# Kernel tuning notes

Hardware: AMD Instinct MI355X
Metric: run time of the kernel (lower is better)

Reference implementation:

```python
import jax, jax.numpy as jnp
import numpy as np

GROUPS = 32
EPS = 1e-5


def setup_inputs() -> dict:
    key = jax.random.key(0)
    ks = jax.random.split(key, 4)
    B, C, H, W = 4, 256, 64, 64
    x = jax.random.normal(ks[0], (B, C, H, W), dtype=jnp.float32)
    gn_w = jnp.ones((C,), jnp.float32)
    gn_b = jnp.zeros((C,), jnp.float32)
    qkv_w = jax.random.normal(ks[1], (3 * C, C), dtype=jnp.float32) * (C ** -0.5)
    qkv_b = jnp.zeros((3 * C,), jnp.float32)
    proj_w = jax.random.normal(ks[2], (C, C), dtype=jnp.float32) * (C ** -0.5)
    proj_b = jnp.zeros((C,), jnp.float32)
    return {"x": x, "gn_w": gn_w, "gn_b": gn_b, "qkv_w": qkv_w,
            "qkv_b": qkv_b, "proj_w": proj_w, "proj_b": proj_b}


def _group_norm(x, w, b):
    B, C, H, W = x.shape
    xr = x.reshape(B, GROUPS, -1)                      # [B, G, (C/G)*H*W]
    mean = xr.mean(axis=-1, keepdims=True)
    var = xr.var(axis=-1, keepdims=True)               # biased, like torch
    h = ((xr - mean) * jax.lax.rsqrt(var + EPS)).reshape(B, C, H, W)
    return h * w[None, :, None, None] + b[None, :, None, None]


def reference(x, gn_w, gn_b, qkv_w, qkv_b, proj_w, proj_b):
    B, C, H, W = x.shape
    h = _group_norm(x, gn_w, gn_b)
    # 1x1 conv == channel GEMM
    qkv = jnp.einsum('oc,bchw->bohw', qkv_w, h) + qkv_b[None, :, None, None]
    qkv = qkv.reshape(B, 3, C, H * W)
    q, k, v = qkv[:, 0], qkv[:, 1], qkv[:, 2]          # [B, C, N]
    scale = C ** (-0.5)
    attn = jax.nn.softmax(jnp.einsum('bci,bcj->bij', q, k) * scale, axis=-1)
    out = jnp.einsum('bij,bcj->bci', attn, v).reshape(B, C, H, W)
    out = jnp.einsum('oc,bchw->bohw', proj_w, out) + proj_b[None, :, None, None]
    return x + out
```

## Files before the change

### kernel.cpp

```cpp
#include <hip/hip_runtime.h>
#include <hip/hip_bf16.h>
#include <math.h>

typedef __bf16 bf16;
typedef __bf16 bf16x8 __attribute__((ext_vector_type(8)));
typedef __bf16 bf16x4 __attribute__((ext_vector_type(4)));
typedef float f32x4 __attribute__((ext_vector_type(4)));
typedef float f32x16 __attribute__((ext_vector_type(16)));

#define MFMA16(a, b, c) __builtin_amdgcn_mfma_f32_16x16x32_bf16(a, b, c, 0, 0, 0)
#define MFMA32(a, b, c) __builtin_amdgcn_mfma_f32_32x32x16_bf16(a, b, c, 0, 0, 0)

#define SCALEK 0.09016844005555896f

typedef const __attribute__((address_space(1))) void* gas_t;
typedef __attribute__((address_space(3))) void* las_t;

__global__ __launch_bounds__(256) void gn_kernel(
    const float* __restrict__ x, const float* __restrict__ gw,
    const float* __restrict__ gb, bf16* __restrict__ h) {
  const int bg = blockIdx.x;
  const int b = bg >> 5, g = bg & 31;
  const size_t base = (size_t)(b * 256 + g * 8) * 4096;
  const float* xp = x + base;
  bf16* hp = h + base;
  const int tid = threadIdx.x;

  float s = 0.f, ss = 0.f;
  for (int i = tid * 4; i < 32768; i += 1024) {
    float4 v = *(const float4*)(xp + i);
    s += v.x + v.y + v.z + v.w;
    ss += v.x * v.x + v.y * v.y + v.z * v.z + v.w * v.w;
  }
#pragma unroll
  for (int off = 32; off; off >>= 1) {
    s += __shfl_down(s, off);
    ss += __shfl_down(ss, off);
  }
  __shared__ float red[8];
  if ((tid & 63) == 0) {
    red[(tid >> 6) * 2] = s;
    red[(tid >> 6) * 2 + 1] = ss;
  }
  __syncthreads();
  s = red[0] + red[2] + red[4] + red[6];
  ss = red[1] + red[3] + red[5] + red[7];
  const float mean = s * (1.f / 32768.f);
  const float var = ss * (1.f / 32768.f) - mean * mean;
  const float rstd = rsqrtf(var + 1e-5f);

  for (int i = tid * 4; i < 32768; i += 1024) {
    float4 v = *(const float4*)(xp + i);
    int c = g * 8 + (i >> 12);
    float a = gw[c] * rstd;
    float b2 = gb[c] - mean * a;
    bf16x4 o;
    o[0] = (bf16)(v.x * a + b2);
    o[1] = (bf16)(v.y * a + b2);
    o[2] = (bf16)(v.z * a + b2);
    o[3] = (bf16)(v.w * a + b2);
    *(bf16x4*)(hp + i) = o;
  }
}

__global__ __launch_bounds__(256) void qkv_gemm(
    const bf16* __restrict__ h, const float* __restrict__ w,
    const float* __restrict__ bias, bf16* __restrict__ qt,
    bf16* __restrict__ kt, bf16* __restrict__ vcm) {
  const int b = blockIdx.z;
  const int o0 = blockIdx.y * 64;
  const int p0 = blockIdx.x * 64;
  __shared__ bf16 Alds[64][56];
  __shared__ bf16 Blds[64][56];
  const int tid = threadIdx.x;
  const int lane = tid & 63, wid = tid >> 6;
  const int lr = lane & 15, lg = lane >> 4;
  const int wm = wid >> 1, wn = wid & 1;
  const bf16* hb = h + (size_t)b * 256 * 4096;

  f32x4 acc[2][2] = {};

  for (int k0 = 0; k0 < 256; k0 += 32) {
    {
      int row = tid >> 2, c8 = (tid & 3) * 8;
      const float* src = w + (size_t)(o0 + row) * 256 + k0 + c8;
      float4 v0 = *(const float4*)src;
      float4 v1 = *(const float4*)(src + 4);
      bf16x8 bv;
      bv[0] = (bf16)v0.x; bv[1] = (bf16)v0.y; bv[2] = (bf16)v0.z; bv[3] = (bf16)v0.w;
      bv[4] = (bf16)v1.x; bv[5] = (bf16)v1.y; bv[6] = (bf16)v1.z; bv[7] = (bf16)v1.w;
      *(bf16x8*)&Alds[row][c8] = bv;
    }
    {
      int cc = tid >> 3, p8 = (tid & 7) * 8;
      bf16x8 v = *(const bf16x8*)(hb + (size_t)(k0 + cc) * 4096 + p0 + p8);
#pragma unroll
      for (int e = 0; e < 8; ++e) Blds[p8 + e][cc] = v[e];
    }
    __syncthreads();
    bf16x8 af[2], bfr[2];
#pragma unroll
    for (int mi = 0; mi < 2; ++mi)
      af[mi] = *(const bf16x8*)&Alds[wm * 32 + mi * 16 + lr][lg * 8];
#pragma unroll
    for (int ni = 0; ni < 2; ++ni)
      bfr[ni] = *(const bf16x8*)&Blds[wn * 32 + ni * 16 + lr][lg * 8];
#pragma unroll
    for (int mi = 0; mi < 2; ++mi)
#pragma unroll
      for (int ni = 0; ni < 2; ++ni)
        acc[mi][ni] = MFMA16(af[mi], bfr[ni], acc[mi][ni]);
    __syncthreads();
  }

#pragma unroll
  for (int mi = 0; mi < 2; ++mi) {
#pragma unroll
    for (int ni = 0; ni < 2; ++ni) {
#pragma unroll
      for (int r = 0; r < 4; ++r) {
        int o = o0 + wm * 32 + mi * 16 + lg * 4 + r;
        int p = p0 + wn * 32 + ni * 16 + lr;
        float val = acc[mi][ni][r] + bias[o];
        if (o < 256) {
          qt[((size_t)b * 4096 + p) * 256 + o] = (bf16)val;
        } else if (o < 512) {
          kt[((size_t)b * 4096 + p) * 256 + (o - 256)] = (bf16)(val * SCALEK);
        } else {
          vcm[((size_t)b * 256 + (o - 512)) * 4096 + p] = (bf16)val;
        }
      }
    }
  }
}

template <int S>
__global__ __launch_bounds__(256, 2) void flash_attn(
    const bf16* __restrict__ qt, const bf16* __restrict__ kt,
    const bf16* __restrict__ vcm, bf16* __restrict__ Opart,
    float* __restrict__ l_g) {
  constexpr int NCOMBO = 4 * S;
  constexpr int CSH = (S == 4) ? 4 : (S == 2) ? 3 : 2;
  constexpr int NIT = (4096 / S) / 32;
  const int bid = blockIdx.x;
  const int combo = bid & (NCOMBO - 1);
  const int qtile = bid >> CSH;
  const int b = combo & 3;
  const int split = combo >> 2;
  const int i0 = qtile * 128;
  const int jbase = split * (4096 / S);

  __shared__ bf16 Klds[2][32][256];
  __shared__ bf16 Vlds[2][256][32];
  const int tid = threadIdx.x;
  const int lane = tid & 63, w = tid >> 6;
  const int ln = lane & 31;
  const int hv = lane >> 5;
  const bf16* qb = qt + (size_t)b * 4096 * 256;
  const bf16* kb = kt + (size_t)b * 4096 * 256;
  const bf16* vb = vcm + (size_t)b * 256 * 4096;

  const int qrow = i0 + w * 32 + ln;
  bf16x8 qf[16];
#pragma unroll
  for (int ks = 0; ks < 16; ++ks)
    qf[ks] = *(const bf16x8*)(qb + (size_t)qrow * 256 + ks * 16 + hv * 8);

  int koff[4], voff[4];
#pragma unroll
  for (int it = 0; it < 4; ++it) {
    int chunk = tid + 256 * it;
    int krow = chunk >> 5;
    koff[it] = krow * 256 + ((((chunk & 31) ^ (krow & 7)) * 8));
    int vrow = chunk >> 2;
    voff[it] = vrow * 4096 + (((chunk & 3) ^ (vrow & 3)) * 8);
  }

#define STAGE(JT, BUF)                                                        \
  {                                                                           \
    const int j0s = jbase + (JT) * 32;                                        \
    _Pragma("unroll") for (int it = 0; it < 4; ++it) {                        \
      int chunk = tid + 256 * it;                                             \
      __builtin_amdgcn_global_load_lds(                                       \
          (gas_t)(const void*)(kb + (size_t)j0s * 256 + koff[it]),            \
          (las_t)(void*)(&Klds[BUF][0][0] + chunk * 8), 16, 0, 0);            \
      __builtin_amdgcn_global_load_lds(                                       \
          (gas_t)(const void*)(vb + (size_t)j0s + voff[it]),                  \
          (las_t)(void*)(&Vlds[BUF][0][0] + chunk * 8), 16, 0, 0);            \
    }                                                                         \
  }

  float llane = 0.f;
  f32x16 accO[8] = {};
  const int kswz = ln & 7;
  const int vswz = ln & 3;

  STAGE(0, 0);
  asm volatile("s_waitcnt vmcnt(0)" ::: "memory");
  __builtin_amdgcn_s_barrier();

  for (int jt = 0; jt < NIT; ++jt) {
    const int cur = jt & 1;
    if (jt + 1 < NIT) STAGE(jt + 1, cur ^ 1);

    f32x16 a0 = {}, a1 = {};
    __builtin_amdgcn_s_setprio(1);
#pragma unroll
    for (int ks = 0; ks < 8; ++ks) {
      bf16x8 kf0 =
          *(const bf16x8*)&Klds[cur][ln][((2 * ks + hv) ^ kswz) * 8];
      bf16x8 kf1 =
          *(const bf16x8*)&Klds[cur][ln][((2 * (ks + 8) + hv) ^ kswz) * 8];
      a0 = MFMA32(kf0, qf[ks], a0);
      a1 = MFMA32(kf1, qf[ks + 8], a1);
    }
    __builtin_amdgcn_s_setprio(0);

    float pv[16];
#pragma unroll
    for (int r = 0; r < 16; ++r) pv[r] = exp2f(a0[r] + a1[r]);
    llane += (((pv[0] + pv[1]) + (pv[2] + pv[3])) +
              ((pv[4] + pv[5]) + (pv[6] + pv[7]))) +
             (((pv[8] + pv[9]) + (pv[10] + pv[11])) +
              ((pv[12] + pv[13]) + (pv[14] + pv[15])));

    int pk[8];
#pragma unroll
    for (int q4 = 0; q4 < 8; ++q4)
      asm("v_cvt_pk_bf16_f32 %0, %1, %2"
          : "=v"(pk[q4])
          : "v"(pv[q4 * 2]), "v"(pv[q4 * 2 + 1]));
    bf16x8 pfrag[2];
#pragma unroll
    for (int s = 0; s < 2; ++s) {
      int xa = pk[s * 4 + 0], ya = pk[s * 4 + 2];
      int xb = pk[s * 4 + 1], yb = pk[s * 4 + 3];
      asm("v_permlane32_swap_b32 %0, %1" : "+v"(xa), "+v"(ya));
      asm("v_permlane32_swap_b32 %0, %1" : "+v"(xb), "+v"(yb));
      union { int i[4]; bf16x8 v; } u;
      u.i[0] = xa; u.i[1] = xb; u.i[2] = ya; u.i[3] = yb;
      pfrag[s] = u.v;
    }

    __builtin_amdgcn_s_setprio(1);
#pragma unroll
    for (int s = 0; s < 2; ++s) {
#pragma unroll
      for (int cb = 0; cb < 8; ++cb) {
        bf16x8 vf =
            *(const bf16x8*)&Vlds[cur][cb * 32 + ln][((2 * s + hv) ^ vswz) * 8];
        accO[cb] = MFMA32(vf, pfrag[s], accO[cb]);
      }
    }
    __builtin_amdgcn_s_setprio(0);

    asm volatile("s_waitcnt vmcnt(0)" ::: "memory");
    __builtin_amdgcn_s_barrier();
  }
#undef STAGE

  bf16* ob = Opart + ((size_t)(split * 4 + b) * 4096 + qrow) * 256;
#pragma unroll
  for (int cb = 0; cb < 8; ++cb) {
#pragma unroll
    for (int g = 0; g < 4; ++g) {
      int lo, hi;
      asm("v_cvt_pk_bf16_f32 %0, %1, %2"
          : "=v"(lo)
          : "v"(accO[cb][g * 4 + 0]), "v"(accO[cb][g * 4 + 1]));
      asm("v_cvt_pk_bf16_f32 %0, %1, %2"
          : "=v"(hi)
          : "v"(accO[cb][g * 4 + 2]), "v"(accO[cb][g * 4 + 3]));
      int2 val; val.x = lo; val.y = hi;
      *(int2*)(ob + cb * 32 + g * 8 + hv * 4) = val;
    }
  }
  {
    int xa = __float_as_int(llane);
    int ya = xa;
    asm("v_permlane32_swap_b32 %0, %1" : "+v"(xa), "+v"(ya));
    float ltot = __int_as_float(xa) + __int_as_float(ya);
    if (hv == 0)
      l_g[(size_t)(split * 4 + b) * 4096 + qrow] = ltot;
  }
}

template <int S>
__global__ __launch_bounds__(256) void merge_kernel(
    const bf16* __restrict__ Opart, const float* __restrict__ l_g,
    bf16* __restrict__ att) {
  int idx = blockIdx.x * 256 + threadIdx.x;
  int row = idx >> 5, c8 = (idx & 31) * 8;
  float L = 0.f;
#pragma unroll
  for (int s = 0; s < S; ++s) L += l_g[s * 16384 + row];
  float acc[8] = {};
#pragma unroll
  for (int s = 0; s < S; ++s) {
    bf16x8 o = *(const bf16x8*)(Opart + ((size_t)s * 16384 + row) * 256 + c8);
#pragma unroll
    for (int e = 0; e < 8; ++e) acc[e] += (float)o[e];
  }
  float inv = 1.f / L;
  bf16x8 res;
#pragma unroll
  for (int e = 0; e < 8; ++e) res[e] = (bf16)(acc[e] * inv);
  *(bf16x8*)(att + (size_t)row * 256 + c8) = res;
}

__global__ __launch_bounds__(256) void proj_gemm(
    const bf16* __restrict__ att, const float* __restrict__ w,
    const float* __restrict__ bias, const float* __restrict__ x,
    float* __restrict__ out) {
  const int b = blockIdx.z;
  const int o0 = blockIdx.y * 64;
  const int p0 = blockIdx.x * 64;
  __shared__ bf16 Alds[64][56];
  __shared__ bf16 Blds[64][56];
  const int tid = threadIdx.x;
  const int lane = tid & 63, wid = tid >> 6;
  const int lr = lane & 15, lg = lane >> 4;
  const int wm = wid >> 1, wn = wid & 1;
  const bf16* ab = att + (size_t)b * 4096 * 256;

  f32x4 acc[2][2] = {};

  for (int k0 = 0; k0 < 256; k0 += 32) {
    {
      int row = tid >> 2, c8 = (tid & 3) * 8;
      const float* src = w + (size_t)(o0 + row) * 256 + k0 + c8;
      float4 v0 = *(const float4*)src;
      float4 v1 = *(const float4*)(src + 4);
      bf16x8 bv;
      bv[0] = (bf16)v0.x; bv[1] = (bf16)v0.y; bv[2] = (bf16)v0.z; bv[3] = (bf16)v0.w;
      bv[4] = (bf16)v1.x; bv[5] = (bf16)v1.y; bv[6] = (bf16)v1.z; bv[7] = (bf16)v1.w;
      *(bf16x8*)&Alds[row][c8] = bv;
    }
    {
      int pr = tid >> 2, c8 = (tid & 3) * 8;
      *(bf16x8*)&Blds[pr][c8] =
          *(const bf16x8*)(ab + (size_t)(p0 + pr) * 256 + k0 + c8);
    }
    __syncthreads();
    bf16x8 af[2], bfr[2];
#pragma unroll
    for (int mi = 0; mi < 2; ++mi)
      af[mi] = *(const bf16x8*)&Alds[wm * 32 + mi * 16 + lr][lg * 8];
#pragma unroll
    for (int ni = 0; ni < 2; ++ni)
      bfr[ni] = *(const bf16x8*)&Blds[wn * 32 + ni * 16 + lr][lg * 8];
#pragma unroll
    for (int mi = 0; mi < 2; ++mi)
#pragma unroll
      for (int ni = 0; ni < 2; ++ni)
        acc[mi][ni] = MFMA16(af[mi], bfr[ni], acc[mi][ni]);
    __syncthreads();
  }

#pragma unroll
  for (int mi = 0; mi < 2; ++mi) {
#pragma unroll
    for (int ni = 0; ni < 2; ++ni) {
#pragma unroll
      for (int r = 0; r < 4; ++r) {
        int o = o0 + wm * 32 + mi * 16 + lg * 4 + r;
        int p = p0 + wn * 32 + ni * 16 + lr;
        size_t idx = ((size_t)b * 256 + o) * 4096 + p;
        out[idx] = acc[mi][ni][r] + bias[o] + x[idx];
      }
    }
  }
}

extern "C" void kernel_launch(void* const* d_in, const int* in_sizes, int n_in,
                              void* d_out, int out_size, void* d_ws,
                              size_t ws_size, hipStream_t stream) {
  (void)in_sizes; (void)n_in; (void)out_size;
  const float* x = (const float*)d_in[0];
  const float* gn_w = (const float*)d_in[1];
  const float* gn_b = (const float*)d_in[2];
  const float* qkv_w = (const float*)d_in[3];
  const float* qkv_b = (const float*)d_in[4];
  const float* proj_w = (const float*)d_in[5];
  const float* proj_b = (const float*)d_in[6];
  float* out = (float*)d_out;

  const size_t MB = 1024ull * 1024ull;
  char* ws = (char*)d_ws;
  bf16* h = (bf16*)(ws);
  bf16* qt = (bf16*)(ws + 8 * MB);
  bf16* kt = (bf16*)(ws + 16 * MB);
  bf16* vcm = (bf16*)(ws + 24 * MB);

  int S;
  if (ws_size >= 32 * MB + 4 * 8 * MB + 4ull * 16384 * sizeof(float)) S = 4;
  else if (ws_size >= 32 * MB + 2 * 8 * MB + 2ull * 16384 * sizeof(float)) S = 2;
  else S = 1;

  bf16* Opart;
  float* l_g;
  bf16* att = h;
  if (S >= 2) {
    Opart = (bf16*)(ws + 32 * MB);
    l_g = (float*)(ws + 32 * MB + (size_t)S * 8 * MB);
  } else {
    Opart = h;
    l_g = (float*)(ws + 32 * MB);
  }

  gn_kernel<<<128, 256, 0, stream>>>(x, gn_w, gn_b, h);
  qkv_gemm<<<dim3(64, 12, 4), 256, 0, stream>>>(h, qkv_w, qkv_b, qt, kt, vcm);
  if (S == 4) {
    flash_attn<4><<<32 * 16, 256, 0, stream>>>(qt, kt, vcm, Opart, l_g);
    merge_kernel<4><<<2048, 256, 0, stream>>>(Opart, l_g, att);
  } else if (S == 2) {
    flash_attn<2><<<32 * 8, 256, 0, stream>>>(qt, kt, vcm, Opart, l_g);
    merge_kernel<2><<<2048, 256, 0, stream>>>(Opart, l_g, att);
  } else {
    flash_attn<1><<<32 * 4, 256, 0, stream>>>(qt, kt, vcm, Opart, l_g);
    merge_kernel<1><<<2048, 256, 0, stream>>>(Opart, l_g, att);
  }
  proj_gemm<<<dim3(64, 4, 4), 256, 0, stream>>>(att, proj_w, proj_b, x, out);
}
```

Measured before the change: 188.8 us.

## Split key tiles across warp pairs in flash attention and fuse merge into projection

Flash attention now uses 64-query tiles. Each pair of warps splits a 64-key tile, and the partial outputs are reduced through LDS at the end. Double-buffered K/V staging is replaced by single buffers whose next-tile loads are issued right after each buffer is consumed, with waits placed between the phases. The separate merge kernel is removed: the projection GEMM now sums the split partials and normalizes by the row sums while loading its B operand. This cuts a kernel launch and the round trip of the merged attention output, in exchange for more blocks, extra barriers and the LDS reduction.

```diff
diff --git a/kernel.cpp b/kernel.cpp
--- a/kernel.cpp
+++ b/kernel.cpp
@@ -141,80 +141,94 @@
     float* __restrict__ l_g) {
   constexpr int NCOMBO = 4 * S;
   constexpr int CSH = (S == 4) ? 4 : (S == 2) ? 3 : 2;
-  constexpr int NIT = (4096 / S) / 32;
+  constexpr int NIT = (4096 / S) / 64;
   const int bid = blockIdx.x;
   const int combo = bid & (NCOMBO - 1);
   const int qtile = bid >> CSH;
   const int b = combo & 3;
   const int split = combo >> 2;
-  const int i0 = qtile * 128;
+  const int i0 = qtile * 64;
   const int jbase = split * (4096 / S);
 
-  __shared__ bf16 Klds[2][32][256];
-  __shared__ bf16 Vlds[2][256][32];
+  __shared__ bf16 Klds[64][256];
+  __shared__ bf16 Vlds[256][64];
+  __shared__ float lred[2][2][32];
   const int tid = threadIdx.x;
   const int lane = tid & 63, w = tid >> 6;
+  const int qg = w >> 1, jg = w & 1;
   const int ln = lane & 31;
   const int hv = lane >> 5;
   const bf16* qb = qt + (size_t)b * 4096 * 256;
   const bf16* kb = kt + (size_t)b * 4096 * 256;
   const bf16* vb = vcm + (size_t)b * 256 * 4096;
 
-  const int qrow = i0 + w * 32 + ln;
+  const int qrow = i0 + qg * 32 + ln;
   bf16x8 qf[16];
 #pragma unroll
   for (int ks = 0; ks < 16; ++ks)
     qf[ks] = *(const bf16x8*)(qb + (size_t)qrow * 256 + ks * 16 + hv * 8);
-
-  int koff[4], voff[4];
-#pragma unroll
-  for (int it = 0; it < 4; ++it) {
+  asm volatile("s_waitcnt vmcnt(0)" ::: "memory");
+
+  int koff[8], voff[8];
+#pragma unroll
+  for (int it = 0; it < 8; ++it) {
     int chunk = tid + 256 * it;
     int krow = chunk >> 5;
-    koff[it] = krow * 256 + ((((chunk & 31) ^ (krow & 7)) * 8));
-    int vrow = chunk >> 2;
-    voff[it] = vrow * 4096 + (((chunk & 3) ^ (vrow & 3)) * 8);
-  }
-
-#define STAGE(JT, BUF)                                                        \
+    int kslot = (chunk & 31) ^ (krow & 7);
+    koff[it] = krow * 256 + kslot * 8;
+    int vrow = chunk >> 3;
+    int vslot = (chunk & 7) ^ (vrow & 7);
+    voff[it] = vrow * 4096 + vslot * 8;
+  }
+
+#define STAGE_K(JT)                                                           \
   {                                                                           \
-    const int j0s = jbase + (JT) * 32;                                        \
-    _Pragma("unroll") for (int it = 0; it < 4; ++it) {                        \
+    const bf16* kbt = kb + (size_t)(jbase + (JT) * 64) * 256;                 \
+    _Pragma("unroll") for (int it = 0; it < 8; ++it) {                        \
       int chunk = tid + 256 * it;                                             \
       __builtin_amdgcn_global_load_lds(                                       \
-          (gas_t)(const void*)(kb + (size_t)j0s * 256 + koff[it]),            \
-          (las_t)(void*)(&Klds[BUF][0][0] + chunk * 8), 16, 0, 0);            \
+          (gas_t)(const void*)(kbt + koff[it]),                               \
+          (las_t)(void*)(&Klds[0][0] + chunk * 8), 16, 0, 0);                 \
+    }                                                                         \
+  }
+#define STAGE_V(JT)                                                           \
+  {                                                                           \
+    const bf16* vbt = vb + (size_t)(jbase + (JT) * 64);                       \
+    _Pragma("unroll") for (int it = 0; it < 8; ++it) {                        \
+      int chunk = tid + 256 * it;                                             \
       __builtin_amdgcn_global_load_lds(                                       \
-          (gas_t)(const void*)(vb + (size_t)j0s + voff[it]),                  \
-          (las_t)(void*)(&Vlds[BUF][0][0] + chunk * 8), 16, 0, 0);            \
+          (gas_t)(const void*)(vbt + voff[it]),                               \
+          (las_t)(void*)(&Vlds[0][0] + chunk * 8), 16, 0, 0);                 \
     }                                                                         \
   }
 
   float llane = 0.f;
   f32x16 accO[8] = {};
-  const int kswz = ln & 7;
-  const int vswz = ln & 3;
-
-  STAGE(0, 0);
-  asm volatile("s_waitcnt vmcnt(0)" ::: "memory");
-  __builtin_amdgcn_s_barrier();
+  const int kk = ln & 7;
+
+  STAGE_K(0);
+  STAGE_V(0);
 
   for (int jt = 0; jt < NIT; ++jt) {
-    const int cur = jt & 1;
-    if (jt + 1 < NIT) STAGE(jt + 1, cur ^ 1);
+    asm volatile("s_waitcnt vmcnt(8)" ::: "memory");
+    __builtin_amdgcn_s_barrier();
+    __builtin_amdgcn_sched_barrier(0);
 
     f32x16 a0 = {}, a1 = {};
     __builtin_amdgcn_s_setprio(1);
 #pragma unroll
     for (int ks = 0; ks < 8; ++ks) {
       bf16x8 kf0 =
-          *(const bf16x8*)&Klds[cur][ln][((2 * ks + hv) ^ kswz) * 8];
+          *(const bf16x8*)&Klds[jg * 32 + ln][((2 * ks + hv) ^ kk) * 8];
       bf16x8 kf1 =
-          *(const bf16x8*)&Klds[cur][ln][((2 * (ks + 8) + hv) ^ kswz) * 8];
+          *(const bf16x8*)&Klds[jg * 32 + ln][((2 * (ks + 8) + hv) ^ kk) * 8];
       a0 = MFMA32(kf0, qf[ks], a0);
       a1 = MFMA32(kf1, qf[ks + 8], a1);
     }
     __builtin_amdgcn_s_setprio(0);
+
+    __builtin_amdgcn_s_barrier();
+    if (jt + 1 < NIT) STAGE_K(jt + 1);
 
     float pv[16];
 #pragma unroll
@@ -223,7 +237,6 @@
               ((pv[4] + pv[5]) + (pv[6] + pv[7]))) +
              (((pv[8] + pv[9]) + (pv[10] + pv[11])) +
               ((pv[12] + pv[13]) + (pv[14] + pv[15])));
-
     int pk[8];
 #pragma unroll
     for (int q4 = 0; q4 < 8; ++q4)
@@ -242,86 +255,122 @@
       pfrag[s] = u.v;
     }
 
+    if (jt + 1 < NIT) {
+      asm volatile("s_waitcnt vmcnt(8)" ::: "memory");
+    } else {
+      asm volatile("s_waitcnt vmcnt(0)" ::: "memory");
+    }
+    __builtin_amdgcn_s_barrier();
+    __builtin_amdgcn_sched_barrier(0);
+
     __builtin_amdgcn_s_setprio(1);
 #pragma unroll
     for (int s = 0; s < 2; ++s) {
 #pragma unroll
       for (int cb = 0; cb < 8; ++cb) {
-        bf16x8 vf =
-            *(const bf16x8*)&Vlds[cur][cb * 32 + ln][((2 * s + hv) ^ vswz) * 8];
+        bf16x8 vf = *(const bf16x8*)&Vlds[cb * 32 + ln]
+                                        [((jg * 4 + s * 2 + hv) ^ kk) * 8];
         accO[cb] = MFMA32(vf, pfrag[s], accO[cb]);
       }
     }
     __builtin_amdgcn_s_setprio(0);
 
-    asm volatile("s_waitcnt vmcnt(0)" ::: "memory");
     __builtin_amdgcn_s_barrier();
-  }
-#undef STAGE
-
-  bf16* ob = Opart + ((size_t)(split * 4 + b) * 4096 + qrow) * 256;
-#pragma unroll
-  for (int cb = 0; cb < 8; ++cb) {
-#pragma unroll
-    for (int g = 0; g < 4; ++g) {
-      int lo, hi;
-      asm("v_cvt_pk_bf16_f32 %0, %1, %2"
-          : "=v"(lo)
-          : "v"(accO[cb][g * 4 + 0]), "v"(accO[cb][g * 4 + 1]));
-      asm("v_cvt_pk_bf16_f32 %0, %1, %2"
-          : "=v"(hi)
-          : "v"(accO[cb][g * 4 + 2]), "v"(accO[cb][g * 4 + 3]));
-      int2 val; val.x = lo; val.y = hi;
-      *(int2*)(ob + cb * 32 + g * 8 + hv * 4) = val;
-    }
-  }
+    if (jt + 1 < NIT) STAGE_V(jt + 1);
+  }
+#undef STAGE_K
+#undef STAGE_V
+
   {
-    int xa = __float_as_int(llane);
-    int ya = xa;
+    int xa = __float_as_int(llane), ya = xa;
     asm("v_permlane32_swap_b32 %0, %1" : "+v"(xa), "+v"(ya));
-    float ltot = __int_as_float(xa) + __int_as_float(ya);
-    if (hv == 0)
-      l_g[(size_t)(split * 4 + b) * 4096 + qrow] = ltot;
+    llane = __int_as_float(xa) + __int_as_float(ya);
+  }
+  if (hv == 0) lred[qg][jg][ln] = llane;
+
+  float* R = (qg == 0) ? (float*)&Klds[0][0] : (float*)&Vlds[0][0];
+#pragma unroll
+  for (int h = 0; h < 2; ++h) {
+    __syncthreads();
+    if (jg == 1) {
+#pragma unroll
+      for (int cb = 0; cb < 4; ++cb) {
+#pragma unroll
+        for (int g = 0; g < 4; ++g) {
+          f32x4 v;
+          v[0] = accO[h * 4 + cb][g * 4 + 0];
+          v[1] = accO[h * 4 + cb][g * 4 + 1];
+          v[2] = accO[h * 4 + cb][g * 4 + 2];
+          v[3] = accO[h * 4 + cb][g * 4 + 3];
+          *(f32x4*)(R + ln * 132 + cb * 32 + g * 8 + hv * 4) = v;
+        }
+      }
+    }
+    __syncthreads();
+    if (jg == 0) {
+#pragma unroll
+      for (int cb = 0; cb < 4; ++cb) {
+#pragma unroll
+        for (int g = 0; g < 4; ++g) {
+          f32x4 v = *(const f32x4*)(R + ln * 132 + cb * 32 + g * 8 + hv * 4);
+          accO[h * 4 + cb][g * 4 + 0] += v[0];
+          accO[h * 4 + cb][g * 4 + 1] += v[1];
+          accO[h * 4 + cb][g * 4 + 2] += v[2];
+          accO[h * 4 + cb][g * 4 + 3] += v[3];
+        }
+      }
+    }
+  }
+  __syncthreads();
+
+  if (jg == 0) {
+    bf16* ob = Opart + ((size_t)(split * 4 + b) * 4096 + qrow) * 256;
+#pragma unroll
+    for (int cb = 0; cb < 8; ++cb) {
+#pragma unroll
+      for (int g = 0; g < 4; ++g) {
+        int lo, hi;
+        asm("v_cvt_pk_bf16_f32 %0, %1, %2"
+            : "=v"(lo)
+            : "v"(accO[cb][g * 4 + 0]), "v"(accO[cb][g * 4 + 1]));
+        asm("v_cvt_pk_bf16_f32 %0, %1, %2"
+            : "=v"(hi)
+            : "v"(accO[cb][g * 4 + 2]), "v"(accO[cb][g * 4 + 3]));
+        int2 val; val.x = lo; val.y = hi;
+        *(int2*)(ob + cb * 32 + g * 8 + hv * 4) = val;
+      }
+    }
+    if (hv == 0) {
+      float lt = lred[qg][0][ln] + lred[qg][1][ln];
+      l_g[(size_t)(split * 4 + b) * 4096 + qrow] = lt;
+    }
   }
 }
 
 template <int S>
-__global__ __launch_bounds__(256) void merge_kernel(
+__global__ __launch_bounds__(256) void proj_fused(
     const bf16* __restrict__ Opart, const float* __restrict__ l_g,
-    bf16* __restrict__ att) {
-  int idx = blockIdx.x * 256 + threadIdx.x;
-  int row = idx >> 5, c8 = (idx & 31) * 8;
-  float L = 0.f;
-#pragma unroll
-  for (int s = 0; s < S; ++s) L += l_g[s * 16384 + row];
-  float acc[8] = {};
-#pragma unroll
-  for (int s = 0; s < S; ++s) {
-    bf16x8 o = *(const bf16x8*)(Opart + ((size_t)s * 16384 + row) * 256 + c8);
-#pragma unroll
-    for (int e = 0; e < 8; ++e) acc[e] += (float)o[e];
-  }
-  float inv = 1.f / L;
-  bf16x8 res;
-#pragma unroll
-  for (int e = 0; e < 8; ++e) res[e] = (bf16)(acc[e] * inv);
-  *(bf16x8*)(att + (size_t)row * 256 + c8) = res;
-}
-
-__global__ __launch_bounds__(256) void proj_gemm(
-    const bf16* __restrict__ att, const float* __restrict__ w,
-    const float* __restrict__ bias, const float* __restrict__ x,
-    float* __restrict__ out) {
+    const float* __restrict__ w, const float* __restrict__ bias,
+    const float* __restrict__ x, float* __restrict__ out) {
   const int b = blockIdx.z;
   const int o0 = blockIdx.y * 64;
   const int p0 = blockIdx.x * 64;
   __shared__ bf16 Alds[64][56];
   __shared__ bf16 Blds[64][56];
+  __shared__ float Linv[64];
   const int tid = threadIdx.x;
   const int lane = tid & 63, wid = tid >> 6;
   const int lr = lane & 15, lg = lane >> 4;
   const int wm = wid >> 1, wn = wid & 1;
-  const bf16* ab = att + (size_t)b * 4096 * 256;
+
+  if (tid < 64) {
+    float L = 0.f;
+#pragma unroll
+    for (int s = 0; s < S; ++s)
+      L += l_g[(size_t)(s * 4 + b) * 4096 + p0 + tid];
+    Linv[tid] = 1.f / L;
+  }
+  __syncthreads();
 
   f32x4 acc[2][2] = {};
 
@@ -338,8 +387,19 @@
     }
     {
       int pr = tid >> 2, c8 = (tid & 3) * 8;
-      *(bf16x8*)&Blds[pr][c8] =
-          *(const bf16x8*)(ab + (size_t)(p0 + pr) * 256 + k0 + c8);
+      float a8[8] = {};
+#pragma unroll
+      for (int s = 0; s < S; ++s) {
+        bf16x8 o = *(const bf16x8*)(
+            Opart + ((size_t)(s * 4 + b) * 4096 + p0 + pr) * 256 + k0 + c8);
+#pragma unroll
+        for (int e = 0; e < 8; ++e) a8[e] += (float)o[e];
+      }
+      float inv = Linv[pr];
+      bf16x8 bv;
+#pragma unroll
+      for (int e = 0; e < 8; ++e) bv[e] = (bf16)(a8[e] * inv);
+      *(bf16x8*)&Blds[pr][c8] = bv;
     }
     __syncthreads();
     bf16x8 af[2], bfr[2];
@@ -397,28 +457,22 @@
   else if (ws_size >= 32 * MB + 2 * 8 * MB + 2ull * 16384 * sizeof(float)) S = 2;
   else S = 1;
 
-  bf16* Opart;
-  float* l_g;
-  bf16* att = h;
-  if (S >= 2) {
-    Opart = (bf16*)(ws + 32 * MB);
-    l_g = (float*)(ws + 32 * MB + (size_t)S * 8 * MB);
-  } else {
-    Opart = h;
-    l_g = (float*)(ws + 32 * MB);
-  }
+  bf16* Opart = (bf16*)(ws + 32 * MB);
+  float* l_g = (float*)(ws + 32 * MB + (size_t)S * 8 * MB);
 
   gn_kernel<<<128, 256, 0, stream>>>(x, gn_w, gn_b, h);
   qkv_gemm<<<dim3(64, 12, 4), 256, 0, stream>>>(h, qkv_w, qkv_b, qt, kt, vcm);
   if (S == 4) {
-    flash_attn<4><<<32 * 16, 256, 0, stream>>>(qt, kt, vcm, Opart, l_g);
-    merge_kernel<4><<<2048, 256, 0, stream>>>(Opart, l_g, att);
+    flash_attn<4><<<64 * 16, 256, 0, stream>>>(qt, kt, vcm, Opart, l_g);
+    proj_fused<4><<<dim3(64, 4, 4), 256, 0, stream>>>(Opart, l_g, proj_w,
+                                                      proj_b, x, out);
   } else if (S == 2) {
-    flash_attn<2><<<32 * 8, 256, 0, stream>>>(qt, kt, vcm, Opart, l_g);
-    merge_kernel<2><<<2048, 256, 0, stream>>>(Opart, l_g, att);
+    flash_attn<2><<<64 * 8, 256, 0, stream>>>(qt, kt, vcm, Opart, l_g);
+    proj_fused<2><<<dim3(64, 4, 4), 256, 0, stream>>>(Opart, l_g, proj_w,
+                                                      proj_b, x, out);
   } else {
-    flash_attn<1><<<32 * 4, 256, 0, stream>>>(qt, kt, vcm, Opart, l_g);
-    merge_kernel<1><<<2048, 256, 0, stream>>>(Opart, l_g, att);
-  }
-  proj_gemm<<<dim3(64, 4, 4), 256, 0, stream>>>(att, proj_w, proj_b, x, out);
+    flash_attn<1><<<64 * 4, 256, 0, stream>>>(qt, kt, vcm, Opart, l_g);
+    proj_fused<1><<<dim3(64, 4, 4), 256, 0, stream>>>(Opart, l_g, proj_w,
+                                                      proj_b, x, out);
+  }
 }
```

Measured after the change: 215.7 us. +14.2%, slower.

## Software-pipeline QK with PV in flash attention and fuse split merge into projection

Applied to the files above, without the earlier changes.

The attention loop is restructured so the QK^T MFMAs for the next key tile interleave with the PV MFMAs of the current tile. K and V staging are split so K runs two tiles ahead and V one tile ahead, with a single wait and barrier at the top of each iteration. The separate merge kernel is removed: the projection GEMM now sums the split partial outputs and divides by the summed row normalisers while loading its B tile. This drops a kernel launch and an intermediate round trip through memory, but the projection repeats the split reduction for each of its four output-channel blocks and holds more registers in the attention loop.

```diff
diff --git a/kernel.cpp b/kernel.cpp
--- a/kernel.cpp
+++ b/kernel.cpp
@@ -176,7 +176,7 @@
     voff[it] = vrow * 4096 + (((chunk & 3) ^ (vrow & 3)) * 8);
   }
 
-#define STAGE(JT, BUF)                                                        \
+#define STAGE_K(JT, BUF)                                                      \
   {                                                                           \
     const int j0s = jbase + (JT) * 32;                                        \
     _Pragma("unroll") for (int it = 0; it < 4; ++it) {                        \
@@ -184,6 +184,13 @@
       __builtin_amdgcn_global_load_lds(                                       \
           (gas_t)(const void*)(kb + (size_t)j0s * 256 + koff[it]),            \
           (las_t)(void*)(&Klds[BUF][0][0] + chunk * 8), 16, 0, 0);            \
+    }                                                                         \
+  }
+#define STAGE_V(JT, BUF)                                                      \
+  {                                                                           \
+    const int j0s = jbase + (JT) * 32;                                        \
+    _Pragma("unroll") for (int it = 0; it < 4; ++it) {                        \
+      int chunk = tid + 256 * it;                                             \
       __builtin_amdgcn_global_load_lds(                                       \
           (gas_t)(const void*)(vb + (size_t)j0s + voff[it]),                  \
           (las_t)(void*)(&Vlds[BUF][0][0] + chunk * 8), 16, 0, 0);            \
@@ -195,26 +202,28 @@
   const int kswz = ln & 7;
   const int vswz = ln & 3;
 
-  STAGE(0, 0);
+  STAGE_K(0, 0);
+  STAGE_V(0, 0);
   asm volatile("s_waitcnt vmcnt(0)" ::: "memory");
   __builtin_amdgcn_s_barrier();
 
-  for (int jt = 0; jt < NIT; ++jt) {
-    const int cur = jt & 1;
-    if (jt + 1 < NIT) STAGE(jt + 1, cur ^ 1);
-
-    f32x16 a0 = {}, a1 = {};
-    __builtin_amdgcn_s_setprio(1);
-#pragma unroll
-    for (int ks = 0; ks < 8; ++ks) {
-      bf16x8 kf0 =
-          *(const bf16x8*)&Klds[cur][ln][((2 * ks + hv) ^ kswz) * 8];
-      bf16x8 kf1 =
-          *(const bf16x8*)&Klds[cur][ln][((2 * (ks + 8) + hv) ^ kswz) * 8];
-      a0 = MFMA32(kf0, qf[ks], a0);
-      a1 = MFMA32(kf1, qf[ks + 8], a1);
-    }
-    __builtin_amdgcn_s_setprio(0);
+  f32x16 a0 = {}, a1 = {};
+#pragma unroll
+  for (int ks = 0; ks < 8; ++ks) {
+    bf16x8 kf0 = *(const bf16x8*)&Klds[0][ln][((2 * ks + hv) ^ kswz) * 8];
+    bf16x8 kf1 =
+        *(const bf16x8*)&Klds[0][ln][((2 * (ks + 8) + hv) ^ kswz) * 8];
+    a0 = MFMA32(kf0, qf[ks], a0);
+    a1 = MFMA32(kf1, qf[ks + 8], a1);
+  }
+  STAGE_K(1, 1);
+
+  for (int t = 0; t < NIT; ++t) {
+    asm volatile("s_waitcnt vmcnt(0)" ::: "memory");
+    __builtin_amdgcn_s_barrier();
+
+    if (t + 1 < NIT) STAGE_V(t + 1, (t + 1) & 1);
+    if (t + 2 < NIT) STAGE_K(t + 2, t & 1);
 
     float pv[16];
 #pragma unroll
@@ -242,22 +251,38 @@
       pfrag[s] = u.v;
     }
 
+    const bf16(*Kc)[256] = Klds[(t + 1) & 1];
+    const bf16(*Vc)[32] = Vlds[t & 1];
     __builtin_amdgcn_s_setprio(1);
-#pragma unroll
-    for (int s = 0; s < 2; ++s) {
-#pragma unroll
-      for (int cb = 0; cb < 8; ++cb) {
-        bf16x8 vf =
-            *(const bf16x8*)&Vlds[cur][cb * 32 + ln][((2 * s + hv) ^ vswz) * 8];
-        accO[cb] = MFMA32(vf, pfrag[s], accO[cb]);
+    if (t + 1 < NIT) {
+      f32x16 n0 = {}, n1 = {};
+#pragma unroll
+      for (int u = 0; u < 8; ++u) {
+        bf16x8 kf0 = *(const bf16x8*)&Kc[ln][((2 * u + hv) ^ kswz) * 8];
+        n0 = MFMA32(kf0, qf[u], n0);
+        bf16x8 kf1 =
+            *(const bf16x8*)&Kc[ln][((2 * (u + 8) + hv) ^ kswz) * 8];
+        n1 = MFMA32(kf1, qf[u + 8], n1);
+        bf16x8 vf0 = *(const bf16x8*)&Vc[u * 32 + ln][((hv) ^ vswz) * 8];
+        accO[u] = MFMA32(vf0, pfrag[0], accO[u]);
+        bf16x8 vf1 = *(const bf16x8*)&Vc[u * 32 + ln][((2 + hv) ^ vswz) * 8];
+        accO[u] = MFMA32(vf1, pfrag[1], accO[u]);
       }
+      a0 = n0;
+      a1 = n1;
+    } else {
+#pragma unroll
+      for (int u = 0; u < 8; ++u) {
+        bf16x8 vf0 = *(const bf16x8*)&Vc[u * 32 + ln][((hv) ^ vswz) * 8];
+        accO[u] = MFMA32(vf0, pfrag[0], accO[u]);
+        bf16x8 vf1 = *(const bf16x8*)&Vc[u * 32 + ln][((2 + hv) ^ vswz) * 8];
+        accO[u] = MFMA32(vf1, pfrag[1], accO[u]);
+      }
     }
     __builtin_amdgcn_s_setprio(0);
-
-    asm volatile("s_waitcnt vmcnt(0)" ::: "memory");
-    __builtin_amdgcn_s_barrier();
-  }
-#undef STAGE
+  }
+#undef STAGE_K
+#undef STAGE_V
 
   bf16* ob = Opart + ((size_t)(split * 4 + b) * 4096 + qrow) * 256;
 #pragma unroll
@@ -286,42 +311,29 @@
 }
 
 template <int S>
-__global__ __launch_bounds__(256) void merge_kernel(
+__global__ __launch_bounds__(256) void proj_fused(
     const bf16* __restrict__ Opart, const float* __restrict__ l_g,
-    bf16* __restrict__ att) {
-  int idx = blockIdx.x * 256 + threadIdx.x;
-  int row = idx >> 5, c8 = (idx & 31) * 8;
-  float L = 0.f;
-#pragma unroll
-  for (int s = 0; s < S; ++s) L += l_g[s * 16384 + row];
-  float acc[8] = {};
-#pragma unroll
-  for (int s = 0; s < S; ++s) {
-    bf16x8 o = *(const bf16x8*)(Opart + ((size_t)s * 16384 + row) * 256 + c8);
-#pragma unroll
-    for (int e = 0; e < 8; ++e) acc[e] += (float)o[e];
-  }
-  float inv = 1.f / L;
-  bf16x8 res;
-#pragma unroll
-  for (int e = 0; e < 8; ++e) res[e] = (bf16)(acc[e] * inv);
-  *(bf16x8*)(att + (size_t)row * 256 + c8) = res;
-}
-
-__global__ __launch_bounds__(256) void proj_gemm(
-    const bf16* __restrict__ att, const float* __restrict__ w,
-    const float* __restrict__ bias, const float* __restrict__ x,
-    float* __restrict__ out) {
+    const float* __restrict__ w, const float* __restrict__ bias,
+    const float* __restrict__ x, float* __restrict__ out) {
   const int b = blockIdx.z;
   const int o0 = blockIdx.y * 64;
   const int p0 = blockIdx.x * 64;
   __shared__ bf16 Alds[64][56];
   __shared__ bf16 Blds[64][56];
+  __shared__ float Linv[64];
   const int tid = threadIdx.x;
   const int lane = tid & 63, wid = tid >> 6;
   const int lr = lane & 15, lg = lane >> 4;
   const int wm = wid >> 1, wn = wid & 1;
-  const bf16* ab = att + (size_t)b * 4096 * 256;
+
+  if (tid < 64) {
+    float L = 0.f;
+#pragma unroll
+    for (int s = 0; s < S; ++s)
+      L += l_g[(size_t)(s * 4 + b) * 4096 + p0 + tid];
+    Linv[tid] = 1.f / L;
+  }
+  __syncthreads();
 
   f32x4 acc[2][2] = {};
 
@@ -338,8 +350,19 @@
     }
     {
       int pr = tid >> 2, c8 = (tid & 3) * 8;
-      *(bf16x8*)&Blds[pr][c8] =
-          *(const bf16x8*)(ab + (size_t)(p0 + pr) * 256 + k0 + c8);
+      float a8[8] = {};
+#pragma unroll
+      for (int s = 0; s < S; ++s) {
+        bf16x8 o = *(const bf16x8*)(
+            Opart + ((size_t)(s * 4 + b) * 4096 + p0 + pr) * 256 + k0 + c8);
+#pragma unroll
+        for (int e = 0; e < 8; ++e) a8[e] += (float)o[e];
+      }
+      float inv = Linv[pr];
+      bf16x8 bv;
+#pragma unroll
+      for (int e = 0; e < 8; ++e) bv[e] = (bf16)(a8[e] * inv);
+      *(bf16x8*)&Blds[pr][c8] = bv;
     }
     __syncthreads();
     bf16x8 af[2], bfr[2];
@@ -397,28 +420,22 @@
   else if (ws_size >= 32 * MB + 2 * 8 * MB + 2ull * 16384 * sizeof(float)) S = 2;
   else S = 1;
 
-  bf16* Opart;
-  float* l_g;
-  bf16* att = h;
-  if (S >= 2) {
-    Opart = (bf16*)(ws + 32 * MB);
-    l_g = (float*)(ws + 32 * MB + (size_t)S * 8 * MB);
-  } else {
-    Opart = h;
-    l_g = (float*)(ws + 32 * MB);
-  }
+  bf16* Opart = (bf16*)(ws + 32 * MB);
+  float* l_g = (float*)(ws + 32 * MB + (size_t)S * 8 * MB);
 
   gn_kernel<<<128, 256, 0, stream>>>(x, gn_w, gn_b, h);
   qkv_gemm<<<dim3(64, 12, 4), 256, 0, stream>>>(h, qkv_w, qkv_b, qt, kt, vcm);
   if (S == 4) {
     flash_attn<4><<<32 * 16, 256, 0, stream>>>(qt, kt, vcm, Opart, l_g);
-    merge_kernel<4><<<2048, 256, 0, stream>>>(Opart, l_g, att);
+    proj_fused<4><<<dim3(64, 4, 4), 256, 0, stream>>>(Opart, l_g, proj_w,
+                                                      proj_b, x, out);
   } else if (S == 2) {
     flash_attn<2><<<32 * 8, 256, 0, stream>>>(qt, kt, vcm, Opart, l_g);
-    merge_kernel<2><<<2048, 256, 0, stream>>>(Opart, l_g, att);
+    proj_fused<2><<<dim3(64, 4, 4), 256, 0, stream>>>(Opart, l_g, proj_w,
+                                                      proj_b, x, out);
   } else {
     flash_attn<1><<<32 * 4, 256, 0, stream>>>(qt, kt, vcm, Opart, l_g);
-    merge_kernel<1><<<2048, 256, 0, stream>>>(Opart, l_g, att);
-  }
-  proj_gemm<<<dim3(64, 4, 4), 256, 0, stream>>>(att, proj_w, proj_b, x, out);
+    proj_fused<1><<<dim3(64, 4, 4), 256, 0, stream>>>(Opart, l_g, proj_w,
+                                                      proj_b, x, out);
+  }
 }
```

After: 178.7 us. -5.3%, faster.
